# Kernel tuning notes

Hardware: AMD Instinct MI355X
Metric: run time of the kernel (lower is better)

Reference implementation:

```python
import jax, jax.numpy as jnp
import numpy as np

N, DEG, FIN, HID, OUT = 50000, 16, 128, 128, 64


def setup_inputs() -> dict:
    key = jax.random.key(0)
    ks = jax.random.split(key, 32)
    x = jax.random.normal(ks[0], (N, FIN), dtype=jnp.float32)
    src = jax.random.randint(ks[1], (N * DEG,), 0, N, dtype=jnp.int32)
    dst = jnp.repeat(jnp.arange(N, dtype=jnp.int32), DEG)  # sorted by target, fixed degree
    edge_index = jnp.stack([src, dst])  # [2, E]
    dims = [(FIN, HID), (HID, HID), (HID, OUT)]
    params = {}
    i = 2
    for l, (fi, fo) in enumerate(dims, 1):
        s_lstm = 1.0 / np.sqrt(fi)
        params[f"W_ih{l}"] = jax.random.normal(ks[i + 0], (4 * fi, fi)) * s_lstm
        params[f"W_hh{l}"] = jax.random.normal(ks[i + 1], (4 * fi, fi)) * s_lstm
        params[f"b_ih{l}"] = jax.random.normal(ks[i + 2], (4 * fi,)) * s_lstm
        params[f"b_hh{l}"] = jax.random.normal(ks[i + 3], (4 * fi,)) * s_lstm
        params[f"Wl{l}"] = jax.random.normal(ks[i + 4], (fo, fi)) * (1.0 / np.sqrt(fi))
        params[f"bl{l}"] = jnp.zeros((fo,), jnp.float32)
        params[f"Wr{l}"] = jax.random.normal(ks[i + 5], (fo, fi)) * (1.0 / np.sqrt(fi))
        i += 6
    return {"x": x, "edge_index": edge_index, **params}


def _lstm_last(neigh, Wih, Whh, bih, bhh):
    # neigh: [N, deg, Fi]; PyTorch LSTM gate order i,f,g,o; return last-step output h.
    h0 = jnp.zeros((neigh.shape[0], Wih.shape[0] // 4), neigh.dtype)
    bias = bih + bhh

    def step(carry, xt):
        h, c = carry
        g = xt @ Wih.T + h @ Whh.T + bias
        i, f, gg, o = jnp.split(g, 4, axis=-1)
        c = jax.nn.sigmoid(f) * c + jax.nn.sigmoid(i) * jnp.tanh(gg)
        h = jax.nn.sigmoid(o) * jnp.tanh(c)
        return (h, c), None

    (h, _), _ = jax.lax.scan(step, (h0, h0), jnp.swapaxes(neigh, 0, 1))
    return h


def _sage_layer(x, src2d, Wih, Whh, bih, bhh, Wl, bl, Wr):
    neigh = x[src2d]  # gather: [N, deg, Fi]
    aggr = _lstm_last(neigh, Wih, Whh, bih, bhh)  # [N, Fi]
    return aggr @ Wl.T + bl + x @ Wr.T  # lin_l(aggr) + lin_r(x)


def reference(x, edge_index,
              W_ih1, W_hh1, b_ih1, b_hh1, Wl1, bl1, Wr1,
              W_ih2, W_hh2, b_ih2, b_hh2, Wl2, bl2, Wr2,
              W_ih3, W_hh3, b_ih3, b_hh3, Wl3, bl3, Wr3):
    n = x.shape[0]
    src2d = edge_index[0].reshape(n, -1)  # fixed-degree, dst-sorted edge list
    h = _sage_layer(x, src2d, W_ih1, W_hh1, b_ih1, b_hh1, Wl1, bl1, Wr1)
    h = jax.nn.relu(h)  # dropout is identity in eval mode
    h = _sage_layer(h, src2d, W_ih2, W_hh2, b_ih2, b_hh2, Wl2, bl2, Wr2)
    h = jax.nn.relu(h)
    return _sage_layer(h, src2d, W_ih3, W_hh3, b_ih3, b_hh3, Wl3, bl3, Wr3)
```

## Files before the change

kernel.cpp:

```cpp
#include <hip/hip_runtime.h>
#include <cstddef>
#include <cstdint>

typedef __attribute__((ext_vector_type(4))) float f32x4;
typedef __attribute__((ext_vector_type(8))) short short8;

#define HID 128
#define NK1 -1.4426950408889634f
#define PK2 2.8853900817779268f

#define BAR_LGKM() __asm__ volatile("s_waitcnt lgkmcnt(0)\ns_barrier" ::: "memory")
#define STEP_BAR2() __asm__ volatile("s_waitcnt vmcnt(2) lgkmcnt(0)\ns_barrier" ::: "memory")

__device__ __forceinline__ short f2bf(float f) {
  unsigned u = __builtin_bit_cast(unsigned, f);
  u += 0x7FFFu + ((u >> 16) & 1u);
  return (short)(u >> 16);
}
__device__ __forceinline__ unsigned pack_bf2(float a, float b) {
  unsigned ua = __builtin_bit_cast(unsigned, a) + 0x8000u;
  unsigned ub = __builtin_bit_cast(unsigned, b) + 0x8000u;
  return __builtin_amdgcn_perm(ub, ua, 0x07060302u);
}
__device__ __forceinline__ float2 unpack2v(int w) {
  float2 r;
  r.x = __builtin_bit_cast(float, (unsigned)(w << 16));
  r.y = __builtin_bit_cast(float, (unsigned)w & 0xffff0000u);
  return r;
}

__device__ __forceinline__ float lstm_elem(float si, float sf, float sg, float so, float& c) {
  float Ei = __builtin_amdgcn_exp2f(si);
  float Ef = __builtin_amdgcn_exp2f(sf);
  float Tg = __builtin_amdgcn_exp2f(sg);
  float Eo = __builtin_amdgcn_exp2f(so);
  float u = 1.0f + Ei, w = 1.0f + Ef, v = Tg + 1.0f, Tm = Tg - 1.0f;
  float t0 = u * v;
  float num = __builtin_fmaf(c, t0, w * Tm);
  float cn = num * __builtin_amdgcn_rcpf(w * t0);
  c = cn;
  float Tc = __builtin_amdgcn_exp2f(PK2 * cn);
  return (Tc - 1.0f) * __builtin_amdgcn_rcpf((1.0f + Eo) * (Tc + 1.0f));
}

__global__ void conv_x_kernel(const float* __restrict__ x, short* __restrict__ xb, int n) {
  int i = blockIdx.x * blockDim.x + threadIdx.x;
  int stride = gridDim.x * blockDim.x;
  for (; i < n; i += stride) xb[i] = f2bf(x[i]);
}

__global__ void conv_layer_kernel(const float* __restrict__ Wih, const float* __restrict__ Whh,
                                  const float* __restrict__ bih, const float* __restrict__ bhh,
                                  const float* __restrict__ Wl, const float* __restrict__ Wr, int foK,
                                  short* __restrict__ wihB, short* __restrict__ whhB,
                                  short* __restrict__ wlB, short* __restrict__ wrB,
                                  float* __restrict__ bsum) {
  int i = blockIdx.x * blockDim.x + threadIdx.x;
  if (i < 512 * HID) {
    float sc = ((i >> 14) == 2) ? PK2 : NK1;
    wihB[i] = f2bf(Wih[i] * sc);
    whhB[i] = f2bf(Whh[i] * sc);
  }
  if (i < foK) { wlB[i] = f2bf(Wl[i]); wrB[i] = f2bf(Wr[i]); }
  if (i < 512) bsum[i] = (bih[i] + bhh[i]) * (((i >> 7) == 2) ? PK2 : NK1);
}

#define OSTR 524
__global__ __launch_bounds__(512, 4) void pgemm_kernel(
    const short* __restrict__ A, const short* __restrict__ W,
    const float* __restrict__ bias, short* __restrict__ out, int M, int ntiles) {
  __shared__ short ldsO[32 * OSTR];
  const int tid = threadIdx.x;
  const int wave = tid >> 6, lane = tid & 63;
  const int quad = lane >> 4, nn = lane & 15;
  const int cbase = wave * 64;

  short8 wreg[4][4];
#pragma unroll
  for (int kt = 0; kt < 4; ++kt)
#pragma unroll
    for (int nt = 0; nt < 4; ++nt)
      wreg[kt][nt] = *(const short8*)(W + (size_t)(cbase + nt * 16 + nn) * HID + kt * 32 + quad * 8);
  f32x4 bias4[4];
#pragma unroll
  for (int nt = 0; nt < 4; ++nt)
#pragma unroll
    for (int r = 0; r < 4; ++r) bias4[nt][r] = bias[cbase + nt * 16 + quad * 4 + r];

#pragma unroll 1
  for (int rt = blockIdx.x; rt < ntiles; rt += gridDim.x) {
    const int row0 = rt * 32;
    f32x4 acc[2][4];
#pragma unroll
    for (int b = 0; b < 2; ++b)
#pragma unroll
      for (int nt = 0; nt < 4; ++nt) acc[b][nt] = bias4[nt];
#pragma unroll
    for (int kt = 0; kt < 4; ++kt) {
      int r0 = row0 + nn;      if (r0 > M - 1) r0 = M - 1;
      int r1 = row0 + 16 + nn; if (r1 > M - 1) r1 = M - 1;
      short8 af0 = *(const short8*)(A + (size_t)r0 * HID + kt * 32 + quad * 8);
      short8 af1 = *(const short8*)(A + (size_t)r1 * HID + kt * 32 + quad * 8);
#pragma unroll
      for (int nt = 0; nt < 4; ++nt) {
        acc[0][nt] = __builtin_amdgcn_mfma_f32_16x16x32_bf16(wreg[kt][nt], af0, acc[0][nt], 0, 0, 0);
        acc[1][nt] = __builtin_amdgcn_mfma_f32_16x16x32_bf16(wreg[kt][nt], af1, acc[1][nt], 0, 0, 0);
      }
    }
    BAR_LGKM();
#pragma unroll
    for (int b = 0; b < 2; ++b)
#pragma unroll
      for (int nt = 0; nt < 4; ++nt) {
        uint2 pk;
        pk.x = pack_bf2(acc[b][nt][0], acc[b][nt][1]);
        pk.y = pack_bf2(acc[b][nt][2], acc[b][nt][3]);
        *(uint2*)(ldsO + (b * 16 + nn) * OSTR + cbase + nt * 16 + quad * 4) = pk;
      }
    BAR_LGKM();
#pragma unroll
    for (int idx = tid; idx < 32 * 64; idx += 512) {
      int row = idx >> 6, c8 = (idx & 63) * 8;
      if (row0 + row < M)
        *(short8*)(out + (size_t)(row0 + row) * 512 + c8) = *(const short8*)(ldsO + row * OSTR + c8);
    }
  }
}

template <int FO, bool RELU, bool OUTF32>
__global__ __launch_bounds__(256, 4) void outgemm_kernel(
    const short* __restrict__ A1, const short* __restrict__ W1,
    const short* __restrict__ A2, const short* __restrict__ W2,
    const float* __restrict__ bias,
    short* __restrict__ outB, float* __restrict__ outF, int M, int ntiles) {
  const int NTW = FO / 64;
  __shared__ char osm[8704];
  short* ldsO = (short*)osm;
  float* ldsF = (float*)osm;
  const int tid = threadIdx.x;
  const int wave = tid >> 6, lane = tid & 63;
  const int quad = lane >> 4, nn = lane & 15;
  const int cbase = wave * (FO / 4);

  short8 w1r[4][NTW], w2r[4][NTW];
#pragma unroll
  for (int kt = 0; kt < 4; ++kt)
#pragma unroll
    for (int nt = 0; nt < NTW; ++nt) {
      w1r[kt][nt] = *(const short8*)(W1 + (size_t)(cbase + nt * 16 + nn) * HID + kt * 32 + quad * 8);
      w2r[kt][nt] = *(const short8*)(W2 + (size_t)(cbase + nt * 16 + nn) * HID + kt * 32 + quad * 8);
    }
  f32x4 bias4[NTW];
#pragma unroll
  for (int nt = 0; nt < NTW; ++nt)
#pragma unroll
    for (int r = 0; r < 4; ++r) bias4[nt][r] = bias[cbase + nt * 16 + quad * 4 + r];

#pragma unroll 1
  for (int rt = blockIdx.x; rt < ntiles; rt += gridDim.x) {
    const int row0 = rt * 32;
    f32x4 acc[2][NTW];
#pragma unroll
    for (int b = 0; b < 2; ++b)
#pragma unroll
      for (int nt = 0; nt < NTW; ++nt) acc[b][nt] = bias4[nt];

#pragma unroll
    for (int kt = 0; kt < 4; ++kt) {
      int r0 = row0 + nn;      if (r0 > M - 1) r0 = M - 1;
      int r1 = row0 + 16 + nn; if (r1 > M - 1) r1 = M - 1;
      short8 a10 = *(const short8*)(A1 + (size_t)r0 * HID + kt * 32 + quad * 8);
      short8 a11 = *(const short8*)(A1 + (size_t)r1 * HID + kt * 32 + quad * 8);
      short8 a20 = *(const short8*)(A2 + (size_t)r0 * HID + kt * 32 + quad * 8);
      short8 a21 = *(const short8*)(A2 + (size_t)r1 * HID + kt * 32 + quad * 8);
#pragma unroll
      for (int nt = 0; nt < NTW; ++nt) {
        acc[0][nt] = __builtin_amdgcn_mfma_f32_16x16x32_bf16(w1r[kt][nt], a10, acc[0][nt], 0, 0, 0);
        acc[1][nt] = __builtin_amdgcn_mfma_f32_16x16x32_bf16(w1r[kt][nt], a11, acc[1][nt], 0, 0, 0);
        acc[0][nt] = __builtin_amdgcn_mfma_f32_16x16x32_bf16(w2r[kt][nt], a20, acc[0][nt], 0, 0, 0);
        acc[1][nt] = __builtin_amdgcn_mfma_f32_16x16x32_bf16(w2r[kt][nt], a21, acc[1][nt], 0, 0, 0);
      }
    }
    BAR_LGKM();
#pragma unroll
    for (int b = 0; b < 2; ++b)
#pragma unroll
      for (int nt = 0; nt < NTW; ++nt) {
        f32x4 v = acc[b][nt];
        if (RELU) {
#pragma unroll
          for (int r = 0; r < 4; ++r) v[r] = fmaxf(v[r], 0.0f);
        }
        int lrow = b * 16 + nn;
        if (OUTF32) {
          *(f32x4*)(ldsF + lrow * 68 + cbase + nt * 16 + quad * 4) = v;
        } else {
          uint2 pk;
          pk.x = pack_bf2(v[0], v[1]);
          pk.y = pack_bf2(v[2], v[3]);
          *(uint2*)(ldsO + lrow * 136 + cbase + nt * 16 + quad * 4) = pk;
        }
      }
    BAR_LGKM();
    if (OUTF32) {
#pragma unroll
      for (int idx = tid; idx < 32 * 16; idx += 256) {
        int row = idx >> 4, c4 = (idx & 15) * 4;
        if (row0 + row < M)
          *(f32x4*)(outF + (size_t)(row0 + row) * 64 + c4) = *(const f32x4*)(ldsF + row * 68 + c4);
      }
    } else {
#pragma unroll
      for (int idx = tid; idx < 32 * 16; idx += 256) {
        int row = idx >> 4, c8 = (idx & 15) * 8;
        if (row0 + row < M)
          *(short8*)(outB + (size_t)(row0 + row) * 128 + c8) = *(const short8*)(ldsO + row * 136 + c8);
      }
    }
  }
}

#define NPB 16
#define PSTR 520
#define HSTR 152
#define LSTM_LDS_BYTES ((3 * NPB * PSTR + 2 * NPB * HSTR) * 2 + 256 * 4)

__global__ __launch_bounds__(512, 4) void lstm_steps_kernel(
    const short* __restrict__ P, const short* __restrict__ Whh,
    const int* __restrict__ src, short* __restrict__ aggr, int M, int ntiles) {
  extern __shared__ char smem[];
  short* Pb = (short*)smem;
  short* Hb = Pb + 3 * NPB * PSTR;
  int* srcL = (int*)(Hb + 2 * NPB * HSTR);

  const int tid = threadIdx.x;
  const int wave = tid >> 6, lane = tid & 63;
  const int quad = lane >> 4, nn = lane & 15;
  const int r0row = wave * 2, r1row = wave * 2 + 1;

  short8 wreg[4][4];
#pragma unroll
  for (int kt = 0; kt < 4; ++kt)
#pragma unroll
    for (int q = 0; q < 4; ++q)
      wreg[kt][q] = *(const short8*)(Whh + (size_t)(q * 128 + wave * 16 + nn) * HID + kt * 32 + quad * 8);

#pragma unroll 1
  for (int tile = blockIdx.x; tile < ntiles; tile += gridDim.x) {
    const int nodeBase = tile * NPB;
    if (tid < 256) {
      int node = nodeBase + (tid >> 4);
      srcL[tid] = (node < M) ? src[nodeBase * 16 + tid] : 0;
    }
    float c_st[4] = {0.f, 0.f, 0.f, 0.f};
    BAR_LGKM();

    {
      int s0A = srcL[r0row * 16 + 0], s0B = srcL[r1row * 16 + 0];
      __builtin_amdgcn_global_load_lds(
          (const __attribute__((address_space(1))) unsigned int*)(P + (size_t)s0A * 512 + lane * 8),
          (__attribute__((address_space(3))) unsigned int*)(Pb + r0row * PSTR), 16, 0, 0);
      __builtin_amdgcn_global_load_lds(
          (const __attribute__((address_space(1))) unsigned int*)(P + (size_t)s0B * 512 + lane * 8),
          (__attribute__((address_space(3))) unsigned int*)(Pb + r1row * PSTR), 16, 0, 0);
      int s1A = srcL[r0row * 16 + 1], s1B = srcL[r1row * 16 + 1];
      __builtin_amdgcn_global_load_lds(
          (const __attribute__((address_space(1))) unsigned int*)(P + (size_t)s1A * 512 + lane * 8),
          (__attribute__((address_space(3))) unsigned int*)(Pb + NPB * PSTR + r0row * PSTR), 16, 0, 0);
      __builtin_amdgcn_global_load_lds(
          (const __attribute__((address_space(1))) unsigned int*)(P + (size_t)s1B * 512 + lane * 8),
          (__attribute__((address_space(3))) unsigned int*)(Pb + NPB * PSTR + r1row * PSTR), 16, 0, 0);
    }
    int sA = srcL[r0row * 16 + 2], sB = srcL[r1row * 16 + 2];

    int pc = 0, pg = 2;
#pragma unroll 1
    for (int t = 0; t < 16; ++t) {
      short* Pc = Pb + pc * NPB * PSTR;
      short* Pg = Pb + pg * NPB * PSTR;
      const short* Hp = Hb + ((t + 1) & 1) * NPB * HSTR;
      short* Hw = Hb + (t & 1) * NPB * HSTR;
      pc = (pc == 2) ? 0 : pc + 1;
      pg = (pg == 2) ? 0 : pg + 1;

      STEP_BAR2();

      const short* pR = Pc + nn * PSTR + wave * 16 + quad * 4;
      uint2 p0 = *(const uint2*)(pR + 0 * 128);
      uint2 p1 = *(const uint2*)(pR + 1 * 128);
      uint2 p2 = *(const uint2*)(pR + 2 * 128);
      uint2 p3 = *(const uint2*)(pR + 3 * 128);
      f32x4 acc[4];
      {
        float2 a0 = unpack2v(p0.x), a1 = unpack2v(p0.y);
        acc[0][0] = a0.x; acc[0][1] = a0.y; acc[0][2] = a1.x; acc[0][3] = a1.y;
        float2 b0 = unpack2v(p1.x), b1 = unpack2v(p1.y);
        acc[1][0] = b0.x; acc[1][1] = b0.y; acc[1][2] = b1.x; acc[1][3] = b1.y;
        float2 c0 = unpack2v(p2.x), c1 = unpack2v(p2.y);
        acc[2][0] = c0.x; acc[2][1] = c0.y; acc[2][2] = c1.x; acc[2][3] = c1.y;
        float2 d0 = unpack2v(p3.x), d1 = unpack2v(p3.y);
        acc[3][0] = d0.x; acc[3][1] = d0.y; acc[3][2] = d1.x; acc[3][3] = d1.y;
      }

      __builtin_amdgcn_global_load_lds(
          (const __attribute__((address_space(1))) unsigned int*)(P + (size_t)sA * 512 + lane * 8),
          (__attribute__((address_space(3))) unsigned int*)(Pg + r0row * PSTR), 16, 0, 0);
      __builtin_amdgcn_global_load_lds(
          (const __attribute__((address_space(1))) unsigned int*)(P + (size_t)sB * 512 + lane * 8),
          (__attribute__((address_space(3))) unsigned int*)(Pg + r1row * PSTR), 16, 0, 0);
      {
        int tn = (t + 3 < 16) ? t + 3 : 15;
        sA = srcL[r0row * 16 + tn];
        sB = srcL[r1row * 16 + tn];
      }

      if (t) {
#pragma unroll
        for (int kt = 0; kt < 4; ++kt) {
          short8 hb = *(const short8*)(Hp + nn * HSTR + kt * 32 + quad * 8);
#pragma unroll
          for (int q = 0; q < 4; ++q)
            acc[q] = __builtin_amdgcn_mfma_f32_16x16x32_bf16(wreg[kt][q], hb, acc[q], 0, 0, 0);
        }
      }

      float hv[4];
#pragma unroll
      for (int r = 0; r < 4; ++r)
        hv[r] = lstm_elem(acc[0][r], acc[1][r], acc[2][r], acc[3][r], c_st[r]);
      uint2 pk;
      pk.x = pack_bf2(hv[0], hv[1]);
      pk.y = pack_bf2(hv[2], hv[3]);
      *(uint2*)(Hw + nn * HSTR + wave * 16 + quad * 4) = pk;
    }

    BAR_LGKM();
    if (tid < 256) {
      int rrow = tid >> 4, off = (tid & 15) * 8;
      int node = nodeBase + rrow;
      if (node < M)
        *(short8*)(aggr + (size_t)node * HID + off) = *(const short8*)(Hb + NPB * HSTR + rrow * HSTR + off);
    }
  }
}

extern "C" void kernel_launch(void* const* d_in, const int* in_sizes, int n_in,
                              void* d_out, int out_size, void* d_ws, size_t ws_size,
                              hipStream_t stream) {
  const float* x = (const float*)d_in[0];
  const int* src = (const int*)d_in[1];
  const float* Wih[3] = {(const float*)d_in[2], (const float*)d_in[9], (const float*)d_in[16]};
  const float* Whh[3] = {(const float*)d_in[3], (const float*)d_in[10], (const float*)d_in[17]};
  const float* bih[3] = {(const float*)d_in[4], (const float*)d_in[11], (const float*)d_in[18]};
  const float* bhh[3] = {(const float*)d_in[5], (const float*)d_in[12], (const float*)d_in[19]};
  const float* Wl[3]  = {(const float*)d_in[6], (const float*)d_in[13], (const float*)d_in[20]};
  const float* bl[3]  = {(const float*)d_in[7], (const float*)d_in[14], (const float*)d_in[21]};
  const float* Wr[3]  = {(const float*)d_in[8], (const float*)d_in[15], (const float*)d_in[22]};

  const int M = in_sizes[0] / HID;

  char* ws = (char*)d_ws;
  size_t off = 0;
  auto alloc = [&](size_t bytes) -> void* {
    void* p = ws + off;
    off += (bytes + 255) & ~(size_t)255;
    return p;
  };
  short* curA = (short*)alloc((size_t)M * HID * 2);
  short* curB = (short*)alloc((size_t)M * HID * 2);
  short* aggr = (short*)alloc((size_t)M * HID * 2);
  short* Pbuf = (short*)alloc((size_t)M * 512 * 2);
  short* wihB[3]; short* whhB[3]; short* wlB[3]; short* wrB[3]; float* bsum[3];
  for (int l = 0; l < 3; ++l) {
    wihB[l] = (short*)alloc(512 * HID * 2);
    whhB[l] = (short*)alloc(512 * HID * 2);
    wlB[l]  = (short*)alloc(HID * HID * 2);
    wrB[l]  = (short*)alloc(HID * HID * 2);
    bsum[l] = (float*)alloc(512 * 4);
  }

  const int nltiles = (M + NPB - 1) / NPB;
  const int ntiles = (M + 31) / 32;

  (void)hipFuncSetAttribute((const void*)lstm_steps_kernel,
                            hipFuncAttributeMaxDynamicSharedMemorySize, LSTM_LDS_BYTES);

  conv_x_kernel<<<2048, 256, 0, stream>>>(x, curA, M * HID);
  for (int l = 0; l < 3; ++l) {
    const int Fo = (l == 2) ? 64 : 128;
    conv_layer_kernel<<<256, 256, 0, stream>>>(Wih[l], Whh[l], bih[l], bhh[l], Wl[l], Wr[l],
                                               Fo * HID, wihB[l], whhB[l], wlB[l], wrB[l], bsum[l]);
  }

  short* cur = curA;
  short* nxt = curB;
  for (int l = 0; l < 3; ++l) {
    pgemm_kernel<<<784, 512, 0, stream>>>(cur, wihB[l], bsum[l], Pbuf, M, ntiles);
    lstm_steps_kernel<<<512, 512, LSTM_LDS_BYTES, stream>>>(Pbuf, whhB[l], src, aggr, M, nltiles);
    if (l < 2) {
      outgemm_kernel<128, true, false><<<784, 256, 0, stream>>>(
          aggr, wlB[l], cur, wrB[l], bl[l], nxt, nullptr, M, ntiles);
      short* tswap = cur; cur = nxt; nxt = tswap;
    } else {
      outgemm_kernel<64, false, true><<<784, 256, 0, stream>>>(
          aggr, wlB[l], cur, wrB[l], bl[l], nullptr, (float*)d_out, M, ntiles);
    }
  }
}
```

Before: 787.4 us.

## Process two node tiles per block in LSTM recurrence to interleave independent chains

```diff
diff --git a/kernel.cpp b/kernel.cpp
--- a/kernel.cpp
+++ b/kernel.cpp
@@ -10,7 +10,7 @@
 #define PK2 2.8853900817779268f
 
 #define BAR_LGKM() __asm__ volatile("s_waitcnt lgkmcnt(0)\ns_barrier" ::: "memory")
-#define STEP_BAR2() __asm__ volatile("s_waitcnt vmcnt(2) lgkmcnt(0)\ns_barrier" ::: "memory")
+#define STEP_BAR4() __asm__ volatile("s_waitcnt vmcnt(4) lgkmcnt(0)\ns_barrier" ::: "memory")
 
 __device__ __forceinline__ short f2bf(float f) {
   unsigned u = __builtin_bit_cast(unsigned, f);
@@ -223,15 +223,17 @@
 #define NPB 16
 #define PSTR 520
 #define HSTR 152
-#define LSTM_LDS_BYTES ((3 * NPB * PSTR + 2 * NPB * HSTR) * 2 + 256 * 4)
-
-__global__ __launch_bounds__(512, 4) void lstm_steps_kernel(
+#define LSTM_LDS_BYTES ((2 * 3 * NPB * PSTR + 2 * 2 * NPB * HSTR) * 2 + 512 * 4)
+
+__global__ __launch_bounds__(512, 2) void lstm_steps_kernel(
     const short* __restrict__ P, const short* __restrict__ Whh,
     const int* __restrict__ src, short* __restrict__ aggr, int M, int ntiles) {
   extern __shared__ char smem[];
-  short* Pb = (short*)smem;
-  short* Hb = Pb + 3 * NPB * PSTR;
-  int* srcL = (int*)(Hb + 2 * NPB * HSTR);
+  short* PbA = (short*)smem;
+  short* PbB = PbA + 3 * NPB * PSTR;
+  short* HbA = PbB + 3 * NPB * PSTR;
+  short* HbB = HbA + 2 * NPB * HSTR;
+  int* srcL = (int*)(HbB + 2 * NPB * HSTR);
 
   const int tid = threadIdx.x;
   const int wave = tid >> 6, lane = tid & 63;
@@ -246,100 +248,147 @@
       wreg[kt][q] = *(const short8*)(Whh + (size_t)(q * 128 + wave * 16 + nn) * HID + kt * 32 + quad * 8);
 
 #pragma unroll 1
-  for (int tile = blockIdx.x; tile < ntiles; tile += gridDim.x) {
-    const int nodeBase = tile * NPB;
-    if (tid < 256) {
-      int node = nodeBase + (tid >> 4);
-      srcL[tid] = (node < M) ? src[nodeBase * 16 + tid] : 0;
-    }
-    float c_st[4] = {0.f, 0.f, 0.f, 0.f};
-    BAR_LGKM();
-
+  for (int tp = blockIdx.x; tp * 2 < ntiles; tp += gridDim.x) {
+    const int tileA = tp * 2;
+    const int tileB = (tp * 2 + 1 < ntiles) ? tp * 2 + 1 : tileA;
     {
-      int s0A = srcL[r0row * 16 + 0], s0B = srcL[r1row * 16 + 0];
-      __builtin_amdgcn_global_load_lds(
-          (const __attribute__((address_space(1))) unsigned int*)(P + (size_t)s0A * 512 + lane * 8),
-          (__attribute__((address_space(3))) unsigned int*)(Pb + r0row * PSTR), 16, 0, 0);
-      __builtin_amdgcn_global_load_lds(
-          (const __attribute__((address_space(1))) unsigned int*)(P + (size_t)s0B * 512 + lane * 8),
-          (__attribute__((address_space(3))) unsigned int*)(Pb + r1row * PSTR), 16, 0, 0);
-      int s1A = srcL[r0row * 16 + 1], s1B = srcL[r1row * 16 + 1];
-      __builtin_amdgcn_global_load_lds(
-          (const __attribute__((address_space(1))) unsigned int*)(P + (size_t)s1A * 512 + lane * 8),
-          (__attribute__((address_space(3))) unsigned int*)(Pb + NPB * PSTR + r0row * PSTR), 16, 0, 0);
-      __builtin_amdgcn_global_load_lds(
-          (const __attribute__((address_space(1))) unsigned int*)(P + (size_t)s1B * 512 + lane * 8),
-          (__attribute__((address_space(3))) unsigned int*)(Pb + NPB * PSTR + r1row * PSTR), 16, 0, 0);
-    }
-    int sA = srcL[r0row * 16 + 2], sB = srcL[r1row * 16 + 2];
+      int which = tid >> 8, idx = tid & 255;
+      int tile = which ? tileB : tileA;
+      int node = tile * NPB + (idx >> 4);
+      srcL[tid] = (node < M) ? src[tile * NPB * 16 + idx] : 0;
+    }
+    float cA[4] = {0.f, 0.f, 0.f, 0.f};
+    float cB[4] = {0.f, 0.f, 0.f, 0.f};
+    const int* sLA = srcL;
+    const int* sLB = srcL + 256;
+    BAR_LGKM();
+
+#pragma unroll
+    for (int tt = 0; tt < 2; ++tt) {
+      {
+        int a0 = sLA[r0row * 16 + tt], a1 = sLA[r1row * 16 + tt];
+        __builtin_amdgcn_global_load_lds(
+            (const __attribute__((address_space(1))) unsigned int*)(P + (size_t)a0 * 512 + lane * 8),
+            (__attribute__((address_space(3))) unsigned int*)(PbA + tt * NPB * PSTR + r0row * PSTR), 16, 0, 0);
+        __builtin_amdgcn_global_load_lds(
+            (const __attribute__((address_space(1))) unsigned int*)(P + (size_t)a1 * 512 + lane * 8),
+            (__attribute__((address_space(3))) unsigned int*)(PbA + tt * NPB * PSTR + r1row * PSTR), 16, 0, 0);
+      }
+      {
+        int b0 = sLB[r0row * 16 + tt], b1 = sLB[r1row * 16 + tt];
+        __builtin_amdgcn_global_load_lds(
+            (const __attribute__((address_space(1))) unsigned int*)(P + (size_t)b0 * 512 + lane * 8),
+            (__attribute__((address_space(3))) unsigned int*)(PbB + tt * NPB * PSTR + r0row * PSTR), 16, 0, 0);
+        __builtin_amdgcn_global_load_lds(
+            (const __attribute__((address_space(1))) unsigned int*)(P + (size_t)b1 * 512 + lane * 8),
+            (__attribute__((address_space(3))) unsigned int*)(PbB + tt * NPB * PSTR + r1row * PSTR), 16, 0, 0);
+      }
+    }
+    int sA0 = sLA[r0row * 16 + 2], sA1 = sLA[r1row * 16 + 2];
+    int sB0 = sLB[r0row * 16 + 2], sB1 = sLB[r1row * 16 + 2];
 
     int pc = 0, pg = 2;
 #pragma unroll 1
     for (int t = 0; t < 16; ++t) {
-      short* Pc = Pb + pc * NPB * PSTR;
-      short* Pg = Pb + pg * NPB * PSTR;
-      const short* Hp = Hb + ((t + 1) & 1) * NPB * HSTR;
-      short* Hw = Hb + (t & 1) * NPB * HSTR;
+      const short* PcA = PbA + pc * NPB * PSTR;
+      const short* PcB = PbB + pc * NPB * PSTR;
+      short* PgA = PbA + pg * NPB * PSTR;
+      short* PgB = PbB + pg * NPB * PSTR;
+      const short* HpA = HbA + ((t + 1) & 1) * NPB * HSTR;
+      const short* HpB = HbB + ((t + 1) & 1) * NPB * HSTR;
+      short* HwA = HbA + (t & 1) * NPB * HSTR;
+      short* HwB = HbB + (t & 1) * NPB * HSTR;
       pc = (pc == 2) ? 0 : pc + 1;
       pg = (pg == 2) ? 0 : pg + 1;
 
-      STEP_BAR2();
-
-      const short* pR = Pc + nn * PSTR + wave * 16 + quad * 4;
-      uint2 p0 = *(const uint2*)(pR + 0 * 128);
-      uint2 p1 = *(const uint2*)(pR + 1 * 128);
-      uint2 p2 = *(const uint2*)(pR + 2 * 128);
-      uint2 p3 = *(const uint2*)(pR + 3 * 128);
-      f32x4 acc[4];
+      STEP_BAR4();
+
+      const short* pRA = PcA + nn * PSTR + wave * 16 + quad * 4;
+      const short* pRB = PcB + nn * PSTR + wave * 16 + quad * 4;
+      uint2 a0 = *(const uint2*)(pRA + 0 * 128);
+      uint2 a1 = *(const uint2*)(pRA + 1 * 128);
+      uint2 a2 = *(const uint2*)(pRA + 2 * 128);
+      uint2 a3 = *(const uint2*)(pRA + 3 * 128);
+      uint2 b0 = *(const uint2*)(pRB + 0 * 128);
+      uint2 b1 = *(const uint2*)(pRB + 1 * 128);
+      uint2 b2 = *(const uint2*)(pRB + 2 * 128);
+      uint2 b3 = *(const uint2*)(pRB + 3 * 128);
+      f32x4 accA[4], accB[4];
       {
-        float2 a0 = unpack2v(p0.x), a1 = unpack2v(p0.y);
-        acc[0][0] = a0.x; acc[0][1] = a0.y; acc[0][2] = a1.x; acc[0][3] = a1.y;
-        float2 b0 = unpack2v(p1.x), b1 = unpack2v(p1.y);
-        acc[1][0] = b0.x; acc[1][1] = b0.y; acc[1][2] = b1.x; acc[1][3] = b1.y;
-        float2 c0 = unpack2v(p2.x), c1 = unpack2v(p2.y);
-        acc[2][0] = c0.x; acc[2][1] = c0.y; acc[2][2] = c1.x; acc[2][3] = c1.y;
-        float2 d0 = unpack2v(p3.x), d1 = unpack2v(p3.y);
-        acc[3][0] = d0.x; acc[3][1] = d0.y; acc[3][2] = d1.x; acc[3][3] = d1.y;
+        float2 u, v;
+        u = unpack2v(a0.x); v = unpack2v(a0.y);
+        accA[0][0] = u.x; accA[0][1] = u.y; accA[0][2] = v.x; accA[0][3] = v.y;
+        u = unpack2v(a1.x); v = unpack2v(a1.y);
+        accA[1][0] = u.x; accA[1][1] = u.y; accA[1][2] = v.x; accA[1][3] = v.y;
+        u = unpack2v(a2.x); v = unpack2v(a2.y);
+        accA[2][0] = u.x; accA[2][1] = u.y; accA[2][2] = v.x; accA[2][3] = v.y;
+        u = unpack2v(a3.x); v = unpack2v(a3.y);
+        accA[3][0] = u.x; accA[3][1] = u.y; accA[3][2] = v.x; accA[3][3] = v.y;
+        u = unpack2v(b0.x); v = unpack2v(b0.y);
+        accB[0][0] = u.x; accB[0][1] = u.y; accB[0][2] = v.x; accB[0][3] = v.y;
+        u = unpack2v(b1.x); v = unpack2v(b1.y);
+        accB[1][0] = u.x; accB[1][1] = u.y; accB[1][2] = v.x; accB[1][3] = v.y;
+        u = unpack2v(b2.x); v = unpack2v(b2.y);
+        accB[2][0] = u.x; accB[2][1] = u.y; accB[2][2] = v.x; accB[2][3] = v.y;
+        u = unpack2v(b3.x); v = unpack2v(b3.y);
+        accB[3][0] = u.x; accB[3][1] = u.y; accB[3][2] = v.x; accB[3][3] = v.y;
       }
 
       __builtin_amdgcn_global_load_lds(
-          (const __attribute__((address_space(1))) unsigned int*)(P + (size_t)sA * 512 + lane * 8),
-          (__attribute__((address_space(3))) unsigned int*)(Pg + r0row * PSTR), 16, 0, 0);
+          (const __attribute__((address_space(1))) unsigned int*)(P + (size_t)sA0 * 512 + lane * 8),
+          (__attribute__((address_space(3))) unsigned int*)(PgA + r0row * PSTR), 16, 0, 0);
       __builtin_amdgcn_global_load_lds(
-          (const __attribute__((address_space(1))) unsigned int*)(P + (size_t)sB * 512 + lane * 8),
-          (__attribute__((address_space(3))) unsigned int*)(Pg + r1row * PSTR), 16, 0, 0);
+          (const __attribute__((address_space(1))) unsigned int*)(P + (size_t)sA1 * 512 + lane * 8),
+          (__attribute__((address_space(3))) unsigned int*)(PgA + r1row * PSTR), 16, 0, 0);
+      __builtin_amdgcn_global_load_lds(
+          (const __attribute__((address_space(1))) unsigned int*)(P + (size_t)sB0 * 512 + lane * 8),
+          (__attribute__((address_space(3))) unsigned int*)(PgB + r0row * PSTR), 16, 0, 0);
+      __builtin_amdgcn_global_load_lds(
+          (const __attribute__((address_space(1))) unsigned int*)(P + (size_t)sB1 * 512 + lane * 8),
+          (__attribute__((address_space(3))) unsigned int*)(PgB + r1row * PSTR), 16, 0, 0);
       {
         int tn = (t + 3 < 16) ? t + 3 : 15;
-        sA = srcL[r0row * 16 + tn];
-        sB = srcL[r1row * 16 + tn];
+        sA0 = sLA[r0row * 16 + tn]; sA1 = sLA[r1row * 16 + tn];
+        sB0 = sLB[r0row * 16 + tn]; sB1 = sLB[r1row * 16 + tn];
       }
 
       if (t) {
 #pragma unroll
         for (int kt = 0; kt < 4; ++kt) {
-          short8 hb = *(const short8*)(Hp + nn * HSTR + kt * 32 + quad * 8);
-#pragma unroll
-          for (int q = 0; q < 4; ++q)
-            acc[q] = __builtin_amdgcn_mfma_f32_16x16x32_bf16(wreg[kt][q], hb, acc[q], 0, 0, 0);
+          short8 hbA = *(const short8*)(HpA + nn * HSTR + kt * 32 + quad * 8);
+          short8 hbB = *(const short8*)(HpB + nn * HSTR + kt * 32 + quad * 8);
+#pragma unroll
+          for (int q = 0; q < 4; ++q) {
+            accA[q] = __builtin_amdgcn_mfma_f32_16x16x32_bf16(wreg[kt][q], hbA, accA[q], 0, 0, 0);
+            accB[q] = __builtin_amdgcn_mfma_f32_16x16x32_bf16(wreg[kt][q], hbB, accB[q], 0, 0, 0);
+          }
         }
       }
 
-      float hv[4];
-#pragma unroll
-      for (int r = 0; r < 4; ++r)
-        hv[r] = lstm_elem(acc[0][r], acc[1][r], acc[2][r], acc[3][r], c_st[r]);
-      uint2 pk;
-      pk.x = pack_bf2(hv[0], hv[1]);
-      pk.y = pack_bf2(hv[2], hv[3]);
-      *(uint2*)(Hw + nn * HSTR + wave * 16 + quad * 4) = pk;
-    }
-
-    BAR_LGKM();
-    if (tid < 256) {
-      int rrow = tid >> 4, off = (tid & 15) * 8;
-      int node = nodeBase + rrow;
+      float hvA[4], hvB[4];
+#pragma unroll
+      for (int r = 0; r < 4; ++r) {
+        hvA[r] = lstm_elem(accA[0][r], accA[1][r], accA[2][r], accA[3][r], cA[r]);
+        hvB[r] = lstm_elem(accB[0][r], accB[1][r], accB[2][r], accB[3][r], cB[r]);
+      }
+      uint2 pkA, pkB;
+      pkA.x = pack_bf2(hvA[0], hvA[1]);
+      pkA.y = pack_bf2(hvA[2], hvA[3]);
+      pkB.x = pack_bf2(hvB[0], hvB[1]);
+      pkB.y = pack_bf2(hvB[2], hvB[3]);
+      *(uint2*)(HwA + nn * HSTR + wave * 16 + quad * 4) = pkA;
+      *(uint2*)(HwB + nn * HSTR + wave * 16 + quad * 4) = pkB;
+    }
+
+    BAR_LGKM();
+    {
+      int which = tid >> 8, idx = tid & 255;
+      int tile = which ? tileB : tileA;
+      const short* Hf = (which ? HbB : HbA) + NPB * HSTR;
+      int rrow = idx >> 4, off = (idx & 15) * 8;
+      int node = tile * NPB + rrow;
       if (node < M)
-        *(short8*)(aggr + (size_t)node * HID + off) = *(const short8*)(Hb + NPB * HSTR + rrow * HSTR + off);
+        *(short8*)(aggr + (size_t)node * HID + off) = *(const short8*)(Hf + rrow * HSTR + off);
     }
   }
 }
```

Result: slower. 931.3 us (+18.3%).

## Fuse output linear layers into LSTM recurrence kernel epilogue

Applied to the files above, without the earlier changes.

```diff
diff --git a/kernel.cpp b/kernel.cpp
--- a/kernel.cpp
+++ b/kernel.cpp
@@ -127,107 +127,18 @@
   }
 }
 
-template <int FO, bool RELU, bool OUTF32>
-__global__ __launch_bounds__(256, 4) void outgemm_kernel(
-    const short* __restrict__ A1, const short* __restrict__ W1,
-    const short* __restrict__ A2, const short* __restrict__ W2,
-    const float* __restrict__ bias,
-    short* __restrict__ outB, float* __restrict__ outF, int M, int ntiles) {
-  const int NTW = FO / 64;
-  __shared__ char osm[8704];
-  short* ldsO = (short*)osm;
-  float* ldsF = (float*)osm;
-  const int tid = threadIdx.x;
-  const int wave = tid >> 6, lane = tid & 63;
-  const int quad = lane >> 4, nn = lane & 15;
-  const int cbase = wave * (FO / 4);
-
-  short8 w1r[4][NTW], w2r[4][NTW];
-#pragma unroll
-  for (int kt = 0; kt < 4; ++kt)
-#pragma unroll
-    for (int nt = 0; nt < NTW; ++nt) {
-      w1r[kt][nt] = *(const short8*)(W1 + (size_t)(cbase + nt * 16 + nn) * HID + kt * 32 + quad * 8);
-      w2r[kt][nt] = *(const short8*)(W2 + (size_t)(cbase + nt * 16 + nn) * HID + kt * 32 + quad * 8);
-    }
-  f32x4 bias4[NTW];
-#pragma unroll
-  for (int nt = 0; nt < NTW; ++nt)
-#pragma unroll
-    for (int r = 0; r < 4; ++r) bias4[nt][r] = bias[cbase + nt * 16 + quad * 4 + r];
-
-#pragma unroll 1
-  for (int rt = blockIdx.x; rt < ntiles; rt += gridDim.x) {
-    const int row0 = rt * 32;
-    f32x4 acc[2][NTW];
-#pragma unroll
-    for (int b = 0; b < 2; ++b)
-#pragma unroll
-      for (int nt = 0; nt < NTW; ++nt) acc[b][nt] = bias4[nt];
-
-#pragma unroll
-    for (int kt = 0; kt < 4; ++kt) {
-      int r0 = row0 + nn;      if (r0 > M - 1) r0 = M - 1;
-      int r1 = row0 + 16 + nn; if (r1 > M - 1) r1 = M - 1;
-      short8 a10 = *(const short8*)(A1 + (size_t)r0 * HID + kt * 32 + quad * 8);
-      short8 a11 = *(const short8*)(A1 + (size_t)r1 * HID + kt * 32 + quad * 8);
-      short8 a20 = *(const short8*)(A2 + (size_t)r0 * HID + kt * 32 + quad * 8);
-      short8 a21 = *(const short8*)(A2 + (size_t)r1 * HID + kt * 32 + quad * 8);
-#pragma unroll
-      for (int nt = 0; nt < NTW; ++nt) {
-        acc[0][nt] = __builtin_amdgcn_mfma_f32_16x16x32_bf16(w1r[kt][nt], a10, acc[0][nt], 0, 0, 0);
-        acc[1][nt] = __builtin_amdgcn_mfma_f32_16x16x32_bf16(w1r[kt][nt], a11, acc[1][nt], 0, 0, 0);
-        acc[0][nt] = __builtin_amdgcn_mfma_f32_16x16x32_bf16(w2r[kt][nt], a20, acc[0][nt], 0, 0, 0);
-        acc[1][nt] = __builtin_amdgcn_mfma_f32_16x16x32_bf16(w2r[kt][nt], a21, acc[1][nt], 0, 0, 0);
-      }
-    }
-    BAR_LGKM();
-#pragma unroll
-    for (int b = 0; b < 2; ++b)
-#pragma unroll
-      for (int nt = 0; nt < NTW; ++nt) {
-        f32x4 v = acc[b][nt];
-        if (RELU) {
-#pragma unroll
-          for (int r = 0; r < 4; ++r) v[r] = fmaxf(v[r], 0.0f);
-        }
-        int lrow = b * 16 + nn;
-        if (OUTF32) {
-          *(f32x4*)(ldsF + lrow * 68 + cbase + nt * 16 + quad * 4) = v;
-        } else {
-          uint2 pk;
-          pk.x = pack_bf2(v[0], v[1]);
-          pk.y = pack_bf2(v[2], v[3]);
-          *(uint2*)(ldsO + lrow * 136 + cbase + nt * 16 + quad * 4) = pk;
-        }
-      }
-    BAR_LGKM();
-    if (OUTF32) {
-#pragma unroll
-      for (int idx = tid; idx < 32 * 16; idx += 256) {
-        int row = idx >> 4, c4 = (idx & 15) * 4;
-        if (row0 + row < M)
-          *(f32x4*)(outF + (size_t)(row0 + row) * 64 + c4) = *(const f32x4*)(ldsF + row * 68 + c4);
-      }
-    } else {
-#pragma unroll
-      for (int idx = tid; idx < 32 * 16; idx += 256) {
-        int row = idx >> 4, c8 = (idx & 15) * 8;
-        if (row0 + row < M)
-          *(short8*)(outB + (size_t)(row0 + row) * 128 + c8) = *(const short8*)(ldsO + row * 136 + c8);
-      }
-    }
-  }
-}
-
 #define NPB 16
 #define PSTR 520
 #define HSTR 152
 #define LSTM_LDS_BYTES ((3 * NPB * PSTR + 2 * NPB * HSTR) * 2 + 256 * 4)
 
-__global__ __launch_bounds__(512, 4) void lstm_steps_kernel(
+template <int FO, bool RELU, bool OUTF32>
+__global__ __launch_bounds__(512, 4) void lstm_fused_kernel(
     const short* __restrict__ P, const short* __restrict__ Whh,
-    const int* __restrict__ src, short* __restrict__ aggr, int M, int ntiles) {
+    const int* __restrict__ src, const short* __restrict__ cur,
+    const short* __restrict__ Wl, const short* __restrict__ Wr,
+    const float* __restrict__ bl,
+    short* __restrict__ outB, float* __restrict__ outF, int M, int ntiles) {
   extern __shared__ char smem[];
   short* Pb = (short*)smem;
   short* Hb = Pb + 3 * NPB * PSTR;
@@ -244,6 +155,12 @@
 #pragma unroll
     for (int q = 0; q < 4; ++q)
       wreg[kt][q] = *(const short8*)(Whh + (size_t)(q * 128 + wave * 16 + nn) * HID + kt * 32 + quad * 8);
+
+  f32x4 biasO = {0.f, 0.f, 0.f, 0.f};
+  if (FO == 128 || wave < 4) {
+#pragma unroll
+    for (int r = 0; r < 4; ++r) biasO[r] = bl[wave * 16 + quad * 4 + r];
+  }
 
 #pragma unroll 1
   for (int tile = blockIdx.x; tile < ntiles; tile += gridDim.x) {
@@ -292,14 +209,15 @@
       uint2 p3 = *(const uint2*)(pR + 3 * 128);
       f32x4 acc[4];
       {
-        float2 a0 = unpack2v(p0.x), a1 = unpack2v(p0.y);
-        acc[0][0] = a0.x; acc[0][1] = a0.y; acc[0][2] = a1.x; acc[0][3] = a1.y;
-        float2 b0 = unpack2v(p1.x), b1 = unpack2v(p1.y);
-        acc[1][0] = b0.x; acc[1][1] = b0.y; acc[1][2] = b1.x; acc[1][3] = b1.y;
-        float2 c0 = unpack2v(p2.x), c1 = unpack2v(p2.y);
-        acc[2][0] = c0.x; acc[2][1] = c0.y; acc[2][2] = c1.x; acc[2][3] = c1.y;
-        float2 d0 = unpack2v(p3.x), d1 = unpack2v(p3.y);
-        acc[3][0] = d0.x; acc[3][1] = d0.y; acc[3][2] = d1.x; acc[3][3] = d1.y;
+        float2 u, v;
+        u = unpack2v(p0.x); v = unpack2v(p0.y);
+        acc[0][0] = u.x; acc[0][1] = u.y; acc[0][2] = v.x; acc[0][3] = v.y;
+        u = unpack2v(p1.x); v = unpack2v(p1.y);
+        acc[1][0] = u.x; acc[1][1] = u.y; acc[1][2] = v.x; acc[1][3] = v.y;
+        u = unpack2v(p2.x); v = unpack2v(p2.y);
+        acc[2][0] = u.x; acc[2][1] = u.y; acc[2][2] = v.x; acc[2][3] = v.y;
+        u = unpack2v(p3.x); v = unpack2v(p3.y);
+        acc[3][0] = u.x; acc[3][1] = u.y; acc[3][2] = v.x; acc[3][3] = v.y;
       }
 
       __builtin_amdgcn_global_load_lds(
@@ -335,11 +253,35 @@
     }
 
     BAR_LGKM();
-    if (tid < 256) {
-      int rrow = tid >> 4, off = (tid & 15) * 8;
-      int node = nodeBase + rrow;
-      if (node < M)
-        *(short8*)(aggr + (size_t)node * HID + off) = *(const short8*)(Hb + NPB * HSTR + rrow * HSTR + off);
+
+    if (FO == 128 || wave < 4) {
+      const short* Hf = Hb + NPB * HSTR;
+      const int cbase = wave * 16;
+      f32x4 accO = biasO;
+#pragma unroll
+      for (int kt = 0; kt < 4; ++kt) {
+        short8 wlA = *(const short8*)(Wl + (size_t)(cbase + nn) * HID + kt * 32 + quad * 8);
+        short8 hb = *(const short8*)(Hf + nn * HSTR + kt * 32 + quad * 8);
+        accO = __builtin_amdgcn_mfma_f32_16x16x32_bf16(wlA, hb, accO, 0, 0, 0);
+        short8 wrA = *(const short8*)(Wr + (size_t)(cbase + nn) * HID + kt * 32 + quad * 8);
+        short8 cb = *(const short8*)(cur + (size_t)(nodeBase + nn) * HID + kt * 32 + quad * 8);
+        accO = __builtin_amdgcn_mfma_f32_16x16x32_bf16(wrA, cb, accO, 0, 0, 0);
+      }
+      if (RELU) {
+#pragma unroll
+        for (int r = 0; r < 4; ++r) accO[r] = fmaxf(accO[r], 0.0f);
+      }
+      int node = nodeBase + nn;
+      if (node < M) {
+        if (OUTF32) {
+          *(f32x4*)(outF + (size_t)node * FO + cbase + quad * 4) = accO;
+        } else {
+          uint2 pko;
+          pko.x = pack_bf2(accO[0], accO[1]);
+          pko.y = pack_bf2(accO[2], accO[3]);
+          *(uint2*)(outB + (size_t)node * FO + cbase + quad * 4) = pko;
+        }
+      }
     }
   }
 }
@@ -368,7 +310,6 @@
   };
   short* curA = (short*)alloc((size_t)M * HID * 2);
   short* curB = (short*)alloc((size_t)M * HID * 2);
-  short* aggr = (short*)alloc((size_t)M * HID * 2);
   short* Pbuf = (short*)alloc((size_t)M * 512 * 2);
   short* wihB[3]; short* whhB[3]; short* wlB[3]; short* wrB[3]; float* bsum[3];
   for (int l = 0; l < 3; ++l) {
@@ -382,7 +323,9 @@
   const int nltiles = (M + NPB - 1) / NPB;
   const int ntiles = (M + 31) / 32;
 
-  (void)hipFuncSetAttribute((const void*)lstm_steps_kernel,
+  (void)hipFuncSetAttribute((const void*)lstm_fused_kernel<128, true, false>,
+                            hipFuncAttributeMaxDynamicSharedMemorySize, LSTM_LDS_BYTES);
+  (void)hipFuncSetAttribute((const void*)lstm_fused_kernel<64, false, true>,
                             hipFuncAttributeMaxDynamicSharedMemorySize, LSTM_LDS_BYTES);
 
   conv_x_kernel<<<2048, 256, 0, stream>>>(x, curA, M * HID);
@@ -396,14 +339,13 @@
   short* nxt = curB;
   for (int l = 0; l < 3; ++l) {
     pgemm_kernel<<<784, 512, 0, stream>>>(cur, wihB[l], bsum[l], Pbuf, M, ntiles);
-    lstm_steps_kernel<<<512, 512, LSTM_LDS_BYTES, stream>>>(Pbuf, whhB[l], src, aggr, M, nltiles);
     if (l < 2) {
-      outgemm_kernel<128, true, false><<<784, 256, 0, stream>>>(
-          aggr, wlB[l], cur, wrB[l], bl[l], nxt, nullptr, M, ntiles);
+      lstm_fused_kernel<128, true, false><<<512, 512, LSTM_LDS_BYTES, stream>>>(
+          Pbuf, whhB[l], src, cur, wlB[l], wrB[l], bl[l], nxt, nullptr, M, nltiles);
       short* tswap = cur; cur = nxt; nxt = tswap;
     } else {
-      outgemm_kernel<64, false, true><<<784, 256, 0, stream>>>(
-          aggr, wlB[l], cur, wrB[l], bl[l], nullptr, (float*)d_out, M, ntiles);
-    }
-  }
-}
+      lstm_fused_kernel<64, false, true><<<512, 512, LSTM_LDS_BYTES, stream>>>(
+          Pbuf, whhB[l], src, cur, wlB[l], wrB[l], bl[l], nullptr, (float*)d_out, M, nltiles);
+    }
+  }
+}
```

After: 764.8 us (median of 2 runs). 1.03x faster.
